# Kernel optimization log

Measured on AMD Instinct MI355X. Metric: run time of the kernel, lower is better.

## Reference

```python
import jax, jax.numpy as jnp
import numpy as np
from jax import lax

TAU = 0.1
LAMBDA_ABCD = 0.5
NUM_ANCHORS = 256
THRESH = 0.6
NEG_INF = -1e30


def sample_features(feat, anchors):
    # feat: [B,C,H,W], anchors: [B,N,2] in [0,1] (u,v). Bilinear, align_corners=False, zeros padding.
    B, C, H, W = feat.shape
    g = anchors * 2.0 - 1.0
    x = ((g[..., 0] + 1.0) * W - 1.0) / 2.0  # [B,N] pixel coords
    y = ((g[..., 1] + 1.0) * H - 1.0) / 2.0
    x0 = jnp.floor(x).astype(jnp.int32); x1 = x0 + 1
    y0 = jnp.floor(y).astype(jnp.int32); y1 = y0 + 1
    wx1 = x - x0.astype(x.dtype); wx0 = 1.0 - wx1
    wy1 = y - y0.astype(y.dtype); wy0 = 1.0 - wy1
    flat = feat.reshape(B, C, H * W)

    def gather(xi, yi):
        valid = ((xi >= 0) & (xi < W) & (yi >= 0) & (yi < H)).astype(feat.dtype)
        idx = jnp.clip(yi, 0, H - 1) * W + jnp.clip(xi, 0, W - 1)  # [B,N]
        v = jnp.take_along_axis(flat, idx[:, None, :], axis=2)  # [B,C,N]
        return v * valid[:, None, :]

    out = (gather(x0, y0) * (wx0 * wy0)[:, None, :]
           + gather(x1, y0) * (wx1 * wy0)[:, None, :]
           + gather(x0, y1) * (wx0 * wy1)[:, None, :]
           + gather(x1, y1) * (wx1 * wy1)[:, None, :])
    return out.transpose(0, 2, 1)  # [B,N,C]


def layer_norm(x, gamma, beta, eps=1e-5):
    mu = x.mean(-1, keepdims=True)
    var = ((x - mu) ** 2).mean(-1, keepdims=True)
    return (x - mu) * lax.rsqrt(var + eps) * gamma + beta


def l2norm(x, eps=1e-12):
    n = jnp.sqrt(jnp.sum(x * x, -1, keepdims=True))
    return x / jnp.maximum(n, eps)


def conv2d(x, w, b, pad):
    y = lax.conv_general_dilated(x, w, (1, 1), pad,
                                 dimension_numbers=('NCHW', 'OIHW', 'NCHW'))
    return y + b[None, :, None, None]


def setup_inputs() -> dict:
    key = jax.random.key(0)
    ks = jax.random.split(key, 12)
    B, Ct, Cs, H, W, P = 16, 1024, 512, 64, 64, 256
    s = lambda k, shp, fan: jax.random.normal(k, shp, jnp.float32) * (1.0 / np.sqrt(fan))
    return {
        'teacher_feat': jax.random.normal(ks[0], (B, Ct, H, W), jnp.float32),
        'student_feat': jax.random.normal(ks[1], (B, Cs, H, W), jnp.float32),
        'conv1_w': s(ks[2], (Ct // 2, Ct, 3, 3), Ct * 9),
        'conv1_b': jnp.zeros((Ct // 2,), jnp.float32),
        'conv2_w': s(ks[3], (1, Ct // 2, 1, 1), Ct // 2),
        'conv2_b': jnp.zeros((1,), jnp.float32),
        't_w': s(ks[4], (Ct, P), Ct), 't_b': jnp.zeros((P,), jnp.float32),
        't_g': jnp.ones((P,), jnp.float32), 't_beta': jnp.zeros((P,), jnp.float32),
        's_w': s(ks[5], (Cs, P), Cs), 's_b': jnp.zeros((P,), jnp.float32),
        's_g': jnp.ones((P,), jnp.float32), 's_beta': jnp.zeros((P,), jnp.float32),
    }


def reference(teacher_feat, student_feat, conv1_w, conv1_b, conv2_w, conv2_b,
              t_w, t_b, t_g, t_beta, s_w, s_b, s_g, s_beta):
    B, Ct, H, W = teacher_feat.shape
    # learnable anchor generator
    h = jax.nn.relu(conv2d(teacher_feat, conv1_w, conv1_b, 'SAME'))
    heatmap = jax.nn.softplus(conv2d(h, conv2_w, conv2_b, 'SAME'))  # [B,1,H,W]
    prob = heatmap.reshape(B, -1)
    prob = prob / (prob.sum(1, keepdims=True) + 1e-6)
    # multinomial without replacement via Gumbel top-k (fixed key -> deterministic)
    u01 = jax.random.uniform(jax.random.key(42), prob.shape, jnp.float32, 1e-8, 1.0)
    gumbel = -jnp.log(-jnp.log(u01))
    idx = lax.top_k(jnp.log(prob + 1e-12) + gumbel, NUM_ANCHORS)[1]  # [B,N]
    ax = (idx % W).astype(jnp.float32) / W
    ay = (idx // W).astype(jnp.float32) / H
    anchors = jnp.stack([ax, ay], -1)  # [B,N,2]

    ft = sample_features(teacher_feat, anchors)  # [B,N,Ct]
    fs = sample_features(student_feat, anchors)  # [B,N,Cs]
    ft = l2norm(layer_norm(jnp.einsum('bnc,cp->bnp', ft, t_w) + t_b, t_g, t_beta))
    fs = l2norm(layer_norm(jnp.einsum('bnc,cp->bnp', fs, s_w) + s_b, s_g, s_beta))

    loss_gafd = jnp.mean((fs - lax.stop_gradient(ft)) ** 2)

    saliency = sample_features(heatmap, anchors)[..., 0]  # [B,N]
    bd = saliency > THRESH * saliency.max(1, keepdims=True)  # [B,N] bool
    non_bd = ~bd

    pos = jnp.sum(fs * ft, -1) / TAU                       # [B,N]
    neg = jnp.einsum('bnc,bmc->bnm', fs, fs) / TAU          # [B,N,N]
    neg = jnp.where(non_bd[:, None, :], neg, NEG_INF)
    logits = jnp.concatenate([pos[..., None], neg], -1)    # [B,N,N+1]
    row_loss = jax.nn.logsumexp(logits, -1) - pos          # [B,N]

    bd_f = bd.astype(jnp.float32)
    cnt = bd_f.sum(1)
    per_b = (row_loss * bd_f).sum(1) / jnp.maximum(cnt, 1.0)
    valid = ((cnt > 0) & (non_bd.sum(1) > 0)).astype(jnp.float32)
    vnum = valid.sum()
    loss_abcd = jnp.where(vnum > 0, (per_b * valid).sum() / jnp.maximum(vnum, 1.0), 0.0)

    total_loss = loss_gafd + LAMBDA_ABCD * loss_abcd
    return total_loss, loss_gafd, loss_abcd, heatmap
```

## Files before the change

kernel.cpp:

```cpp
#include <hip/hip_runtime.h>
#include <stdint.h>


typedef float f32x4 __attribute__((ext_vector_type(4)));
typedef short s16x8 __attribute__((ext_vector_type(8)));

__device__ __forceinline__ unsigned short f2bf(float f) {
  unsigned u = __float_as_uint(f);
  u += 0x7fffu + ((u >> 16) & 1u);
  return (unsigned short)(u >> 16);
}
__device__ __forceinline__ float bf2f(unsigned short h) {
  return __uint_as_float((unsigned)h << 16);
}

__device__ __forceinline__ void gld16(const void* g, void* l) {
  __builtin_amdgcn_global_load_lds(
      (const __attribute__((address_space(1))) void*)g,
      (__attribute__((address_space(3))) void*)l, 16, 0, 0);
}

__device__ __forceinline__ float block_sum(float v, float* l4) {
  for (int m = 32; m; m >>= 1) v += __shfl_xor(v, m, 64);
  int wid = threadIdx.x >> 6;
  if ((threadIdx.x & 63) == 0) l4[wid] = v;
  __syncthreads();
  float r = l4[0] + l4[1] + l4[2] + l4[3];
  __syncthreads();
  return r;
}

__global__ void k_pad_transpose(const float* __restrict__ teacher,
                                unsigned short* __restrict__ tpad) {
  __shared__ __align__(16) unsigned short lds[64 * 65];
  int bid = blockIdx.x;
  int cb = bid & 15, y = (bid >> 4) & 63, b = bid >> 10;
  int t = threadIdx.x;
#pragma unroll
  for (int it = 0; it < 4; ++it) {
    int idx = it * 256 + t;
    int cl = idx >> 4, x4 = (idx & 15) * 4;
    float4 v = *(const float4*)&teacher[(size_t)(b * 1024 + cb * 64 + cl) * 4096 + y * 64 + x4];
    lds[cl * 65 + x4 + 0] = f2bf(v.x);
    lds[cl * 65 + x4 + 1] = f2bf(v.y);
    lds[cl * 65 + x4 + 2] = f2bf(v.z);
    lds[cl * 65 + x4 + 3] = f2bf(v.w);
  }
  __syncthreads();
  size_t obase = ((size_t)(b * 66 + y + 1) * 66 + 1) * 1024 + cb * 64;
#pragma unroll
  for (int it = 0; it < 2; ++it) {
    int wi = it * 256 + t;
    int x = wi >> 3, c0 = (wi & 7) * 8;
    s16x8 v;
#pragma unroll
    for (int k2 = 0; k2 < 8; ++k2) v[k2] = (short)lds[(c0 + k2) * 65 + x];
    *(s16x8*)(void*)&tpad[obase + (size_t)x * 1024 + c0] = v;
  }
  if (y == 0) {
    for (int idx = t; idx < 66 * 64; idx += 256) {
      int col = idx >> 6, cl = idx & 63;
      tpad[((size_t)(b * 66) * 66 + col) * 1024 + cb * 64 + cl] = 0;
    }
  }
  if (y == 63) {
    for (int idx = t; idx < 66 * 64; idx += 256) {
      int col = idx >> 6, cl = idx & 63;
      tpad[((size_t)(b * 66 + 65) * 66 + col) * 1024 + cb * 64 + cl] = 0;
    }
  }
  if (t < 128) {
    int col = (t >= 64) ? 65 : 0;
    int cl = t & 63;
    tpad[((size_t)(b * 66 + y + 1) * 66 + col) * 1024 + cb * 64 + cl] = 0;
  }
}

__global__ void k_wprep_all(const float* __restrict__ w1,
                            unsigned short* __restrict__ wt,
                            const float* __restrict__ tw, unsigned short* __restrict__ wTt,
                            const float* __restrict__ sw, unsigned short* __restrict__ wTs) {
  int blk = blockIdx.x, t = threadIdx.x;
  if (blk < 512) {
    __shared__ float wl[9216];
    int co = blk;
    const float* src = w1 + (size_t)co * 9216;
    for (int i = t; i < 9216; i += 256) wl[i] = src[i];
    __syncthreads();
    for (int i = t; i < 9216; i += 256) {
      int tap = i >> 10;
      int ci = i - (tap << 10);
      int kb = ci >> 6, kc = ci & 63;
      wt[(size_t)tap * 524288 + (size_t)kb * 32768 + co * 64 + kc] = f2bf(wl[ci * 9 + tap]);
    }
  } else if (blk < 1536) {
    int e = (blk - 512) * 256 + t;
    int p = e >> 10, k = e & 1023;
    wTt[e] = f2bf(tw[(size_t)k * 256 + p]);
  } else {
    int e = (blk - 1536) * 256 + t;
    int p = e >> 9, k = e & 511;
    wTs[e] = f2bf(sw[(size_t)k * 256 + p]);
  }
}

#define STAGE_A(buf, ts, h) do {                                              \
    int tap_ = (ts) >> 4, kb_ = (ts) & 15;                                    \
    int ky_ = tap_ / 3, kx_ = tap_ - ky_ * 3;                                 \
    unsigned o_ = (unsigned)(((ky_ * 66 + kx_) << 10) + (kb_ << 6));          \
    gld16(tpad + aoff[(h) * 2 + 0] + o_,                                      \
          (char*)(As[buf] + (((h) * 128 + wid * 8) << 6)));                   \
    gld16(tpad + aoff[(h) * 2 + 1] + o_,                                      \
          (char*)(As[buf] + (((h) * 128 + 64 + wid * 8) << 6)));              \
  } while (0)

#define STAGE_B(buf, ts, h) do {                                              \
    int tap_ = (ts) >> 4, kb_ = (ts) & 15;                                    \
    unsigned o_ = (unsigned)((tap_ << 19) + (kb_ << 15));                     \
    gld16(wt + boff[(h) * 2 + 0] + o_,                                        \
          (char*)(Bs[buf] + (((h) * 128 + wid * 8) << 6)));                   \
    gld16(wt + boff[(h) * 2 + 1] + o_,                                        \
          (char*)(Bs[buf] + (((h) * 128 + 64 + wid * 8) << 6)));              \
  } while (0)

#define LDA8(AF, buf, i0)                                                     \
  _Pragma("unroll") for (int i_ = 0; i_ < 4; ++i_)                            \
  _Pragma("unroll") for (int s_ = 0; s_ < 2; ++s_)                            \
    AF[i_][s_] = *(const s16x8*)(const void*)(                                \
        &As[buf][(wm * 128 + ((i0) + i_) * 16 + l15) * 64 +                   \
                 ((s_ * 4 + quad) ^ sw7) * 8]);

#define LDB4(BF, buf, j0)                                                     \
  _Pragma("unroll") for (int j_ = 0; j_ < 2; ++j_)                            \
  _Pragma("unroll") for (int s_ = 0; s_ < 2; ++s_)                            \
    BF[j_][s_] = *(const s16x8*)(const void*)(                                \
        &Bs[buf][(wn * 64 + ((j0) + j_) * 16 + l15) * 64 +                    \
                 ((s_ * 4 + quad) ^ sw7) * 8]);

#define MFMA16(AF, BF, i0, j0)                                                \
  _Pragma("unroll") for (int i_ = 0; i_ < 4; ++i_)                            \
  _Pragma("unroll") for (int j_ = 0; j_ < 2; ++j_)                            \
  _Pragma("unroll") for (int s_ = 0; s_ < 2; ++s_)                            \
    acc[(i0) + i_][(j0) + j_] = __builtin_amdgcn_mfma_f32_16x16x32_bf16(      \
        AF[i_][s_], BF[j_][s_], acc[(i0) + i_][(j0) + j_], 0, 0, 0);

#define PHASE_MID()                                                           \
  __builtin_amdgcn_s_barrier();                                               \
  asm volatile("s_waitcnt lgkmcnt(0)" ::: "memory");                          \
  __builtin_amdgcn_sched_barrier(0);                                          \
  __builtin_amdgcn_s_setprio(1)

#define PHASE_END()                                                           \
  __builtin_amdgcn_s_setprio(0);                                              \
  __builtin_amdgcn_sched_barrier(0);                                          \
  __builtin_amdgcn_s_barrier()

#define PHASE_END_VM()                                                        \
  __builtin_amdgcn_s_setprio(0);                                              \
  __builtin_amdgcn_sched_barrier(0);                                          \
  asm volatile("s_waitcnt vmcnt(4)" ::: "memory");                            \
  __builtin_amdgcn_s_barrier()

__global__ __launch_bounds__(512, 2) void k_conv(
    const unsigned short* __restrict__ tpad, const unsigned short* __restrict__ wt,
    const float* __restrict__ b1, const float* __restrict__ w2,
    float* __restrict__ heat) {
  __shared__ __align__(16) unsigned short As[2][256 * 64];
  __shared__ __align__(16) unsigned short Bs[2][256 * 64];
  int bid = blockIdx.x;
  int swz = (bid & 7) * 64 + (bid >> 3);
  int nt = swz & 1, mt = swz >> 1;
  int m0 = mt * 256, n0 = nt * 256;
  int t = threadIdx.x, wid = t >> 6, lane = t & 63;
  int wm = wid >> 2, wn = wid & 3;
  int quad = lane >> 4, l15 = lane & 15;
  int sw7 = l15 & 7;

  int srcChunk = (t & 7) ^ ((t >> 3) & 7);
  unsigned aoff[4], boff[4];
#pragma unroll
  for (int v = 0; v < 4; ++v) {
    int row = (v >> 1) * 128 + (v & 1) * 64 + (t >> 3);
    int m = m0 + row;
    int b = m >> 12, y = (m >> 6) & 63, x = m & 63;
    aoff[v] = (unsigned)((((b * 66 + y) * 66 + x) << 10) + srcChunk * 8);
    boff[v] = (unsigned)(((n0 + row) << 6) + srcChunk * 8);
  }

  f32x4 acc[8][4];
  const f32x4 fz = {0.f, 0.f, 0.f, 0.f};
#pragma unroll
  for (int i = 0; i < 8; ++i)
#pragma unroll
    for (int j = 0; j < 4; ++j) acc[i][j] = fz;

  STAGE_B(0, 0, 0); STAGE_B(0, 0, 1);
  STAGE_A(0, 0, 0); STAGE_A(0, 0, 1);
  STAGE_B(1, 1, 0); STAGE_B(1, 1, 1);
  asm volatile("s_waitcnt vmcnt(4)" ::: "memory");
  __builtin_amdgcn_s_barrier();

  for (int it2 = 0; it2 < 72; ++it2) {
    int T1 = it2 * 2 + 1;
    int tsA = (T1 + 1 <= 143) ? T1 + 1 : 143;
    int tsB = (T1 + 2 <= 143) ? T1 + 2 : 143;
    s16x8 af[4][2], bf01[2][2], bf23[2][2];
    LDA8(af, 0, 0);
    LDB4(bf01, 0, 0);
    STAGE_A(1, T1, 0);
    PHASE_MID();
    MFMA16(af, bf01, 0, 0);
    LDB4(bf23, 0, 2);
    PHASE_END();

    STAGE_A(1, T1, 1);
    PHASE_MID();
    MFMA16(af, bf23, 0, 2);
    LDA8(af, 0, 4);
    PHASE_END();

    STAGE_B(0, tsA, 0);
    PHASE_MID();
    MFMA16(af, bf01, 4, 0);
    PHASE_END();

    STAGE_B(0, tsA, 1);
    PHASE_MID();
    MFMA16(af, bf23, 4, 2);
    PHASE_END_VM();

    LDA8(af, 1, 0);
    LDB4(bf01, 1, 0);
    STAGE_A(0, tsA, 0);
    PHASE_MID();
    MFMA16(af, bf01, 0, 0);
    LDB4(bf23, 1, 2);
    PHASE_END();

    STAGE_A(0, tsA, 1);
    PHASE_MID();
    MFMA16(af, bf23, 0, 2);
    LDA8(af, 1, 4);
    PHASE_END();

    STAGE_B(1, tsB, 0);
    PHASE_MID();
    MFMA16(af, bf01, 4, 0);
    PHASE_END();

    STAGE_B(1, tsB, 1);
    PHASE_MID();
    MFMA16(af, bf23, 4, 2);
    PHASE_END_VM();
  }

  float w2v[4], b1v[4];
#pragma unroll
  for (int j = 0; j < 4; ++j) {
    int co = n0 + wn * 64 + j * 16 + l15;
    w2v[j] = w2[co];
    b1v[j] = b1[co];
  }
#pragma unroll
  for (int i = 0; i < 8; ++i) {
#pragma unroll
    for (int r = 0; r < 4; ++r) {
      float part = 0.f;
#pragma unroll
      for (int j = 0; j < 4; ++j) {
        float v = acc[i][j][r] + b1v[j];
        v = fmaxf(v, 0.f);
        part += v * w2v[j];
      }
#pragma unroll
      for (int msk = 1; msk < 16; msk <<= 1) part += __shfl_xor(part, msk, 64);
      if (l15 == 0) atomicAdd(&heat[m0 + wm * 128 + i * 16 + quad * 4 + r], part);
    }
  }
}

__device__ __forceinline__ unsigned rotl32(unsigned x, int d) {
  return (x << d) | (x >> (32 - d));
}
__device__ unsigned threefry_bits(unsigned lo) {
  const unsigned k0 = 0u, k1 = 42u;
  const unsigned k2 = 0x1BD11BDAu ^ k0 ^ k1;
  unsigned x0 = 0u + k0, x1 = lo + k1;
#define TF_R4(a, bq, c, d)                                \
  x0 += x1; x1 = rotl32(x1, a); x1 ^= x0;                 \
  x0 += x1; x1 = rotl32(x1, bq); x1 ^= x0;                \
  x0 += x1; x1 = rotl32(x1, c); x1 ^= x0;                 \
  x0 += x1; x1 = rotl32(x1, d); x1 ^= x0;
  TF_R4(13, 15, 26, 6)  x0 += k1; x1 += k2 + 1u;
  TF_R4(17, 29, 16, 24) x0 += k2; x1 += k0 + 2u;
  TF_R4(13, 15, 26, 6)  x0 += k0; x1 += k1 + 3u;
  TF_R4(17, 29, 16, 24) x0 += k1; x1 += k2 + 4u;
  TF_R4(13, 15, 26, 6)  x0 += k2; x1 += k0 + 5u;
#undef TF_R4
  return x0 ^ x1;
}

__global__ void k_score_topk_sal(const float* __restrict__ heat,
                                 const float* __restrict__ b2p,
                                 float* __restrict__ out_hm,
                                 int* __restrict__ idx_sel,
                                 int* __restrict__ bd, int* __restrict__ cnt,
                                 int* __restrict__ nbc) {
  __shared__ float hmp[4096];
  __shared__ unsigned keys[4096];
  __shared__ unsigned hist[256];
  __shared__ unsigned suf[256];
  __shared__ unsigned sel[2];
  __shared__ int wpos;
  __shared__ int idxl[256];
  __shared__ float l4[4];
  int b = blockIdx.x, t = threadIdx.x;
  float b2 = b2p[0];
  float lsum = 0.f;
#pragma unroll
  for (int j = 0; j < 16; ++j) {
    int e = j * 256 + t;
    float x = heat[b * 4096 + e] + b2;
    float sp = fmaxf(x, 0.f) + log1pf(expf(-fabsf(x)));
    hmp[e] = sp;
    lsum += sp;
  }
  float S = block_sum(lsum, l4);
  float denom = S + 1e-6f;
#pragma unroll
  for (int j = 0; j < 16; ++j) {
    int e = j * 256 + t;
    float sp = hmp[e];
    out_hm[b * 4096 + e] = sp;
    float lp = logf(sp / denom + 1e-12f);
    unsigned bits = threefry_bits((unsigned)(b * 4096 + e));
    float u01 = __uint_as_float((bits >> 9) | 0x3f800000u) - 1.0f;
    float u = fmaxf(1e-8f, u01 * (1.0f - 1e-8f) + 1e-8f);
    float gum = -logf(-logf(u));
    float sc = lp + gum;
    unsigned uu = __float_as_uint(sc);
    uu = (uu >> 31) ? ~uu : (uu | 0x80000000u);
    keys[e] = uu;
  }
  if (t == 0) wpos = 0;
  unsigned prefix = 0, hmask = 0, r = 256;
  for (int pass = 0; pass < 4; ++pass) {
    int shift = 24 - 8 * pass;
    hist[t] = 0;
    __syncthreads();
#pragma unroll
    for (int j = 0; j < 16; ++j) {
      unsigned u = keys[j * 256 + t];
      if ((u & hmask) == prefix) atomicAdd(&hist[(u >> shift) & 255u], 1u);
    }
    __syncthreads();
    suf[t] = hist[t];
    __syncthreads();
    for (int off = 1; off < 256; off <<= 1) {
      unsigned v = (t + off < 256) ? suf[t + off] : 0u;
      __syncthreads();
      suf[t] += v;
      __syncthreads();
    }
    unsigned above = (t < 255) ? suf[t + 1] : 0u;
    if (suf[t] >= r && above < r) {
      sel[0] = (unsigned)t;
      sel[1] = above;
    }
    __syncthreads();
    prefix |= sel[0] << shift;
    hmask |= 0xFFu << shift;
    r -= sel[1];
    __syncthreads();
  }
#pragma unroll
  for (int j = 0; j < 16; ++j) {
    int e = j * 256 + t;
    if (keys[e] > prefix) {
      int s = atomicAdd(&wpos, 1);
      idx_sel[b * 256 + s] = e;
      idxl[s] = e;
    }
  }
  __syncthreads();
#pragma unroll
  for (int j = 0; j < 16; ++j) {
    int e = j * 256 + t;
    if (keys[e] == prefix) {
      int s = atomicAdd(&wpos, 1);
      if (s < 256) {
        idx_sel[b * 256 + s] = e;
        idxl[s] = e;
      }
    }
  }
  __syncthreads();
  int idx = idxl[t];
  int px = idx & 63, py = idx >> 6;
  float v = 0.f;
  if (py > 0) {
    if (px > 0) v += hmp[(py - 1) * 64 + px - 1];
    v += hmp[(py - 1) * 64 + px];
  }
  if (px > 0) v += hmp[py * 64 + px - 1];
  v += hmp[py * 64 + px];
  float sal = 0.25f * v;
  float mx = sal;
  for (int m = 32; m; m >>= 1) mx = fmaxf(mx, __shfl_xor(mx, m, 64));
  if ((t & 63) == 0) l4[t >> 6] = mx;
  __syncthreads();
  mx = fmaxf(fmaxf(l4[0], l4[1]), fmaxf(l4[2], l4[3]));
  __syncthreads();
  int bdv = sal > 0.6f * mx ? 1 : 0;
  bd[b * 256 + t] = bdv;
  float c = block_sum((float)bdv, l4);
  if (t == 0) {
    cnt[b] = (int)c;
    nbc[b] = 256 - (int)c;
  }
}

__global__ void k_gather_t(const unsigned short* __restrict__ tpad,
                           const int* __restrict__ idx_sel,
                           unsigned short* __restrict__ ftb) {
  int t = threadIdx.x;
  int bn = blockIdx.x * 2 + (t >> 7);
  int tt = t & 127;
  int b = bn >> 8;
  int idx = idx_sel[bn];
  int px = idx & 63, py = idx >> 6;
  const unsigned short* base = tpad + ((size_t)(b * 66 + py) * 66 + px) * 1024 + tt * 8;
  s16x8 r0 = *(const s16x8*)(const void*)(base);
  s16x8 r1 = *(const s16x8*)(const void*)(base + 1024);
  s16x8 r2 = *(const s16x8*)(const void*)(base + 66 * 1024);
  s16x8 r3 = *(const s16x8*)(const void*)(base + 67 * 1024);
  s16x8 o;
#pragma unroll
  for (int k = 0; k < 8; ++k) {
    float v = bf2f((unsigned short)r0[k]) + bf2f((unsigned short)r1[k]) +
              bf2f((unsigned short)r2[k]) + bf2f((unsigned short)r3[k]);
    o[k] = (short)f2bf(0.25f * v);
  }
  *(s16x8*)(void*)&ftb[(size_t)bn * 1024 + tt * 8] = o;
}

__global__ void k_gather_s(const float* __restrict__ student,
                           const int* __restrict__ idx_sel,
                           unsigned short* __restrict__ fsbT) {
  __shared__ float plane[4096];
  int blk = blockIdx.x;
  int b = blk >> 9, c = blk & 511;
  int t = threadIdx.x;
  const float4* g4 = (const float4*)(student + ((size_t)b * 512 + c) * 4096);
  float4* p4 = (float4*)plane;
  for (int i = t; i < 1024; i += 256) p4[i] = g4[i];
  __syncthreads();
  int idx = idx_sel[b * 256 + t];
  int px = idx & 63, py = idx >> 6;
  float v = 0.f;
  if (py > 0) {
    if (px > 0) v += plane[(py - 1) * 64 + px - 1];
    v += plane[(py - 1) * 64 + px];
  }
  if (px > 0) v += plane[py * 64 + px - 1];
  v += plane[py * 64 + px];
  fsbT[((size_t)b * 512 + c) * 256 + t] = f2bf(0.25f * v);
}

__global__ void k_fsb_tr(const unsigned short* __restrict__ fsbT,
                         unsigned short* __restrict__ fsb) {
  __shared__ unsigned short tile[64][65];
  int blk = blockIdx.x;
  int b = blk >> 5, ct = (blk >> 2) & 7, nt = blk & 3;
  int t = threadIdx.x;
#pragma unroll
  for (int it = 0; it < 16; ++it) {
    int e = it * 256 + t;
    int cl = e >> 6, n = e & 63;
    tile[cl][n] = fsbT[((size_t)(b * 512 + ct * 64 + cl)) * 256 + nt * 64 + n];
  }
  __syncthreads();
#pragma unroll
  for (int it = 0; it < 16; ++it) {
    int e = it * 256 + t;
    int n = e >> 6, cl = e & 63;
    fsb[((size_t)(b * 256 + nt * 64 + n)) * 512 + ct * 64 + cl] = tile[cl][n];
  }
}

__global__ __launch_bounds__(256) void k_proj_both(
    const unsigned short* __restrict__ At, const unsigned short* __restrict__ Wtt,
    const unsigned short* __restrict__ Asrc, const unsigned short* __restrict__ Wts,
    float* __restrict__ outt, float* __restrict__ outs) {
  __shared__ __align__(16) unsigned short Al[128 * 64];
  __shared__ __align__(16) unsigned short Bl[128 * 64];
  int g = blockIdx.x;
  const unsigned short* A;
  const unsigned short* Wt;
  float* outp;
  int K, bid;
  if (g < 64) { A = At; Wt = Wtt; outp = outt; K = 1024; bid = g; }
  else        { A = Asrc; Wt = Wts; outp = outs; K = 512; bid = g - 64; }
  int nt = bid & 1, mt = bid >> 1;
  int m0 = mt * 128, n0 = nt * 128;
  int t = threadIdx.x, wid = t >> 6, lane = t & 63;
  int wm = wid & 1, wn = wid >> 1;
  int quad = lane >> 4, l15 = lane & 15;

  f32x4 acc[4][4];
  const f32x4 fz = {0.f, 0.f, 0.f, 0.f};
#pragma unroll
  for (int i = 0; i < 4; ++i)
#pragma unroll
    for (int j = 0; j < 4; ++j) acc[i][j] = fz;

  int row4[4];
#pragma unroll
  for (int jj = 0; jj < 4; ++jj) row4[jj] = (wid * 4 + jj) * 8 + (lane >> 3);
  int kcol = (lane & 7) * 8;

  int nkb = K >> 6;
  for (int kb = 0; kb < nkb; ++kb) {
#pragma unroll
    for (int jj = 0; jj < 4; ++jj) {
      gld16(A + (size_t)(m0 + row4[jj]) * K + kb * 64 + kcol,
            (char*)Al + (wid * 4 + jj) * 1024);
      gld16(Wt + (size_t)(n0 + row4[jj]) * K + kb * 64 + kcol,
            (char*)Bl + (wid * 4 + jj) * 1024);
    }
    __syncthreads();
#pragma unroll
    for (int s = 0; s < 2; ++s) {
      s16x8 af[4], bf[4];
#pragma unroll
      for (int i = 0; i < 4; ++i) {
        af[i] = *(const s16x8*)(const void*)(Al + (wm * 64 + i * 16 + l15) * 64 + s * 32 + quad * 8);
        bf[i] = *(const s16x8*)(const void*)(Bl + (wn * 64 + i * 16 + l15) * 64 + s * 32 + quad * 8);
      }
#pragma unroll
      for (int i = 0; i < 4; ++i)
#pragma unroll
        for (int j = 0; j < 4; ++j)
          acc[i][j] = __builtin_amdgcn_mfma_f32_16x16x32_bf16(af[i], bf[j], acc[i][j], 0, 0, 0);
    }
    __syncthreads();
  }
#pragma unroll
  for (int i = 0; i < 4; ++i)
#pragma unroll
    for (int j = 0; j < 4; ++j)
#pragma unroll
      for (int r = 0; r < 4; ++r) {
        int m = m0 + wm * 64 + i * 16 + quad * 4 + r;
        int p = n0 + wn * 64 + j * 16 + l15;
        outp[(size_t)m * 256 + p] = acc[i][j][r];
      }
}

__global__ void k_ln(const float* __restrict__ projp, const float* __restrict__ bias,
                     const float* __restrict__ g, const float* __restrict__ beta,
                     float* __restrict__ outf) {
  __shared__ float l4[4];
  int row = blockIdx.x, t = threadIdx.x;
  float x = projp[(size_t)row * 256 + t] + bias[t];
  float s1 = block_sum(x, l4);
  float mu = s1 * (1.f / 256.f);
  float d = x - mu;
  float s2 = block_sum(d * d, l4);
  float rstd = rsqrtf(s2 * (1.f / 256.f) + 1e-5f);
  float xn = d * rstd * g[t] + beta[t];
  float ss = block_sum(xn * xn, l4);
  float o = xn / fmaxf(sqrtf(ss), 1e-12f);
  outf[(size_t)row * 256 + t] = o;
}

__global__ void k_ln_s_pos(const float* __restrict__ projp, const float* __restrict__ bias,
                           const float* __restrict__ g, const float* __restrict__ beta,
                           const float* __restrict__ ftn,
                           float* __restrict__ outf, unsigned short* __restrict__ outb,
                           float* __restrict__ pos, float* __restrict__ gsum) {
  __shared__ float l4[4];
  int row = blockIdx.x, t = threadIdx.x;
  float x = projp[(size_t)row * 256 + t] + bias[t];
  float s1 = block_sum(x, l4);
  float mu = s1 * (1.f / 256.f);
  float d = x - mu;
  float s2 = block_sum(d * d, l4);
  float rstd = rsqrtf(s2 * (1.f / 256.f) + 1e-5f);
  float xn = d * rstd * g[t] + beta[t];
  float ss = block_sum(xn * xn, l4);
  float o = xn / fmaxf(sqrtf(ss), 1e-12f);
  outf[(size_t)row * 256 + t] = o;
  outb[(size_t)row * 256 + t] = f2bf(o);
  float bt = ftn[(size_t)row * 256 + t];
  float sdot = block_sum(o * bt, l4);
  if (t == 0) pos[row] = sdot * 10.f;
  float dd = o - bt;
  float ssq = block_sum(dd * dd, l4);
  if (t == 0) atomicAdd(gsum, ssq);
}

__global__ __launch_bounds__(256) void k_abcd_rows(
    const unsigned short* __restrict__ fsnb, const int* __restrict__ bd,
    const float* __restrict__ pos, float* __restrict__ rowloss) {
  __shared__ __align__(16) unsigned short Ab[64 * 64];
  __shared__ __align__(16) unsigned short Bb[256 * 64];
  __shared__ float mrg[64][4][2];
  int b = blockIdx.x >> 2, nb = blockIdx.x & 3;
  int n0 = nb * 64;
  int t = threadIdx.x, w = t >> 6, lane = t & 63, quad = lane >> 4, l15 = lane & 15;
  f32x4 acc[4][4];
  const f32x4 fz = {0.f, 0.f, 0.f, 0.f};
#pragma unroll
  for (int i = 0; i < 4; ++i)
#pragma unroll
    for (int j = 0; j < 4; ++j) acc[i][j] = fz;
  const unsigned short* fb = fsnb + (size_t)b * 256 * 256;

  for (int kc = 0; kc < 4; ++kc) {
    {
      int r = t >> 2, cc = (t & 3) * 16;
      const uint4* s = (const uint4*)(const void*)(fb + (size_t)(n0 + r) * 256 + kc * 64 + cc);
      *(uint4*)(void*)(Ab + r * 64 + cc) = s[0];
      *(uint4*)(void*)(Ab + r * 64 + cc + 8) = s[1];
    }
#pragma unroll
    for (int it = 0; it < 4; ++it) {
      int m = it * 64 + (t >> 2), cc = (t & 3) * 16;
      const uint4* s = (const uint4*)(const void*)(fb + (size_t)m * 256 + kc * 64 + cc);
      *(uint4*)(void*)(Bb + m * 64 + cc) = s[0];
      *(uint4*)(void*)(Bb + m * 64 + cc + 8) = s[1];
    }
    __syncthreads();
#pragma unroll
    for (int s = 0; s < 2; ++s) {
      s16x8 af[4], bf[4];
#pragma unroll
      for (int i = 0; i < 4; ++i) {
        af[i] = *(const s16x8*)(const void*)(Ab + (i * 16 + l15) * 64 + s * 32 + quad * 8);
        bf[i] = *(const s16x8*)(const void*)(Bb + (w * 64 + i * 16 + l15) * 64 + s * 32 + quad * 8);
      }
#pragma unroll
      for (int i = 0; i < 4; ++i)
#pragma unroll
        for (int j = 0; j < 4; ++j)
          acc[i][j] = __builtin_amdgcn_mfma_f32_16x16x32_bf16(af[i], bf[j], acc[i][j], 0, 0, 0);
    }
    __syncthreads();
  }

  int nbmask[4];
#pragma unroll
  for (int j = 0; j < 4; ++j) nbmask[j] = bd[b * 256 + w * 64 + j * 16 + l15];
#pragma unroll
  for (int i = 0; i < 4; ++i) {
#pragma unroll
    for (int r = 0; r < 4; ++r) {
      float mxv = -1e30f, se = 0.f;
#pragma unroll
      for (int j = 0; j < 4; ++j) {
        float v = nbmask[j] ? -1e30f : (acc[i][j][r] / 0.1f);
        if (v > mxv) {
          se = se * expf(mxv - v) + 1.f;
          mxv = v;
        } else {
          se += expf(v - mxv);
        }
      }
#pragma unroll
      for (int msk = 1; msk < 16; msk <<= 1) {
        float omx = __shfl_xor(mxv, msk, 64);
        float ose = __shfl_xor(se, msk, 64);
        float nm = fmaxf(mxv, omx);
        se = se * expf(mxv - nm) + ose * expf(omx - nm);
        mxv = nm;
      }
      if (l15 == 0) {
        mrg[i * 16 + quad * 4 + r][w][0] = mxv;
        mrg[i * 16 + quad * 4 + r][w][1] = se;
      }
    }
  }
  __syncthreads();
  if (t < 64) {
    float MX = -1e30f, SE = 0.f;
    for (int ww = 0; ww < 4; ++ww) {
      float omx = mrg[t][ww][0], ose = mrg[t][ww][1];
      float nm = fmaxf(MX, omx);
      SE = SE * expf(MX - nm) + ose * expf(omx - nm);
      MX = nm;
    }
    float p = pos[b * 256 + n0 + t];
    float nm = fmaxf(MX, p);
    float se2 = SE * expf(MX - nm) + expf(p - nm);
    rowloss[b * 256 + n0 + t] = nm + logf(se2) - p;
  }
}

__global__ void k_final(const float* __restrict__ gsum, const float* __restrict__ rowloss,
                        const int* __restrict__ bd, const int* __restrict__ cnt,
                        const int* __restrict__ nbc, float* __restrict__ out) {
  __shared__ float l4[4];
  int t = threadIdx.x;
  float abcd_acc = 0.f, vnum = 0.f;
  for (int b = 0; b < 16; ++b) {
    float c = bd[b * 256 + t] ? rowloss[b * 256 + t] : 0.f;
    float s = block_sum(c, l4);
    if (t == 0) {
      float cb = (float)cnt[b];
      float per = s / fmaxf(cb, 1.f);
      if (cnt[b] > 0 && nbc[b] > 0) {
        abcd_acc += per;
        vnum += 1.f;
      }
    }
  }
  if (t == 0) {
    float gafd = gsum[0] / 1048576.f;
    float abcd = vnum > 0.f ? abcd_acc / fmaxf(vnum, 1.f) : 0.f;
    out[0] = gafd + 0.5f * abcd;
    out[1] = gafd;
    out[2] = abcd;
  }
}

static constexpr size_t OFF_TPAD = 0;
static constexpr size_t TPAD_BYTES = (size_t)16 * 66 * 66 * 1024 * 2;
static constexpr size_t OFF_WT = OFF_TPAD + TPAD_BYTES;
static constexpr size_t WT_BYTES = (size_t)9 * 16 * 512 * 64 * 2;
static constexpr size_t OFF_HEAT = OFF_WT + WT_BYTES;
static constexpr size_t OFF_GSUM = OFF_HEAT + 262144;
static constexpr size_t OFF_HM = OFF_GSUM + 256;
static constexpr size_t OFF_SC = OFF_HM + 262144;
static constexpr size_t OFF_IDX = OFF_SC + 262144;
static constexpr size_t OFF_FTB = OFF_IDX + 16384;
static constexpr size_t OFF_FSB = OFF_FTB + (size_t)4096 * 1024 * 2;
static constexpr size_t OFF_FSBT = OFF_FSB + (size_t)4096 * 512 * 2;
static constexpr size_t OFF_WTT = OFF_FSBT + (size_t)4096 * 512 * 2;
static constexpr size_t OFF_WTS = OFF_WTT + (size_t)256 * 1024 * 2;
static constexpr size_t OFF_PRT = OFF_WTS + (size_t)256 * 512 * 2;
static constexpr size_t OFF_PRS = OFF_PRT + (size_t)4096 * 256 * 4;
static constexpr size_t OFF_FTN = OFF_PRS + (size_t)4096 * 256 * 4;
static constexpr size_t OFF_FSN = OFF_FTN + (size_t)4096 * 256 * 4;
static constexpr size_t OFF_FSNB = OFF_FSN + (size_t)4096 * 256 * 4;
static constexpr size_t OFF_POS = OFF_FSNB + (size_t)4096 * 256 * 2;
static constexpr size_t OFF_BD = OFF_POS + 16384;
static constexpr size_t OFF_CNT = OFF_BD + 16384;
static constexpr size_t OFF_NBC = OFF_CNT + 64;
static constexpr size_t OFF_RL = OFF_NBC + 64;

extern "C" void kernel_launch(void* const* d_in, const int* in_sizes, int n_in,
                              void* d_out, int out_size, void* d_ws, size_t ws_size,
                              hipStream_t stream) {
  const float* teacher = (const float*)d_in[0];
  const float* student = (const float*)d_in[1];
  const float* w1 = (const float*)d_in[2];
  const float* b1 = (const float*)d_in[3];
  const float* w2 = (const float*)d_in[4];
  const float* b2 = (const float*)d_in[5];
  const float* t_w = (const float*)d_in[6];
  const float* t_b = (const float*)d_in[7];
  const float* t_g = (const float*)d_in[8];
  const float* t_be = (const float*)d_in[9];
  const float* s_w = (const float*)d_in[10];
  const float* s_b = (const float*)d_in[11];
  const float* s_g = (const float*)d_in[12];
  const float* s_be = (const float*)d_in[13];
  float* out = (float*)d_out;

  char* ws = (char*)d_ws;
  unsigned short* tpad = (unsigned short*)(ws + OFF_TPAD);
  unsigned short* wt = (unsigned short*)(ws + OFF_WT);
  float* heat = (float*)(ws + OFF_HEAT);
  float* gsum = (float*)(ws + OFF_GSUM);
  int* idx_sel = (int*)(ws + OFF_IDX);
  unsigned short* ftb = (unsigned short*)(ws + OFF_FTB);
  unsigned short* fsb = (unsigned short*)(ws + OFF_FSB);
  unsigned short* fsbT = (unsigned short*)(ws + OFF_FSBT);
  unsigned short* wTt = (unsigned short*)(ws + OFF_WTT);
  unsigned short* wTs = (unsigned short*)(ws + OFF_WTS);
  float* projt = (float*)(ws + OFF_PRT);
  float* projs = (float*)(ws + OFF_PRS);
  float* ftn = (float*)(ws + OFF_FTN);
  float* fsn = (float*)(ws + OFF_FSN);
  unsigned short* fsnb = (unsigned short*)(ws + OFF_FSNB);
  float* pos = (float*)(ws + OFF_POS);
  int* bd = (int*)(ws + OFF_BD);
  int* cnt = (int*)(ws + OFF_CNT);
  int* nbc = (int*)(ws + OFF_NBC);
  float* rowloss = (float*)(ws + OFF_RL);

  hipMemsetAsync(ws + OFF_HEAT, 0, 262144 + 256, stream);

  k_pad_transpose<<<16384, 256, 0, stream>>>(teacher, tpad);
  k_wprep_all<<<2048, 256, 0, stream>>>(w1, wt, t_w, wTt, s_w, wTs);
  k_conv<<<512, 512, 0, stream>>>(tpad, wt, b1, w2, heat);
  k_score_topk_sal<<<16, 256, 0, stream>>>(heat, b2, out + 3, idx_sel, bd, cnt, nbc);
  k_gather_t<<<2048, 256, 0, stream>>>(tpad, idx_sel, ftb);
  k_gather_s<<<8192, 256, 0, stream>>>(student, idx_sel, fsbT);
  k_fsb_tr<<<512, 256, 0, stream>>>(fsbT, fsb);
  k_proj_both<<<128, 256, 0, stream>>>(ftb, wTt, fsb, wTs, projt, projs);
  k_ln<<<4096, 256, 0, stream>>>(projt, t_b, t_g, t_be, ftn);
  k_ln_s_pos<<<4096, 256, 0, stream>>>(projs, s_b, s_g, s_be, ftn, fsn, fsnb, pos, gsum);
  k_abcd_rows<<<64, 256, 0, stream>>>(fsnb, bd, pos, rowloss);
  k_final<<<1, 256, 0, stream>>>(gsum, rowloss, bd, cnt, nbc, out);
}
```

Measured before the change: 1.144 ms.

## Merge pad and weight-prep kernels, reschedule conv loop, warp-scan histogram, split abcd rows

Fuses the teacher pad/transpose and weight-prep kernels into a single launch that shares one LDS buffer, removing one kernel launch. In the conv main loop, the A-stage loads are issued before the LDS reads, with sched_barrier and setprio hints replacing one PHASE_MID. The top-k histogram suffix sum switches from a barrier-heavy LDS scan to a wave-shuffle scan. The ABCD row kernel uses 32-row tiles over twice as many blocks to raise parallelism, at the cost of reloading the B tile more often.

```diff
diff --git a/kernel.cpp b/kernel.cpp
--- a/kernel.cpp
+++ b/kernel.cpp
@@ -30,60 +30,58 @@
   return r;
 }
 
-__global__ void k_pad_transpose(const float* __restrict__ teacher,
-                                unsigned short* __restrict__ tpad) {
-  __shared__ __align__(16) unsigned short lds[64 * 65];
-  int bid = blockIdx.x;
-  int cb = bid & 15, y = (bid >> 4) & 63, b = bid >> 10;
-  int t = threadIdx.x;
-#pragma unroll
-  for (int it = 0; it < 4; ++it) {
-    int idx = it * 256 + t;
-    int cl = idx >> 4, x4 = (idx & 15) * 4;
-    float4 v = *(const float4*)&teacher[(size_t)(b * 1024 + cb * 64 + cl) * 4096 + y * 64 + x4];
-    lds[cl * 65 + x4 + 0] = f2bf(v.x);
-    lds[cl * 65 + x4 + 1] = f2bf(v.y);
-    lds[cl * 65 + x4 + 2] = f2bf(v.z);
-    lds[cl * 65 + x4 + 3] = f2bf(v.w);
-  }
-  __syncthreads();
-  size_t obase = ((size_t)(b * 66 + y + 1) * 66 + 1) * 1024 + cb * 64;
-#pragma unroll
-  for (int it = 0; it < 2; ++it) {
-    int wi = it * 256 + t;
-    int x = wi >> 3, c0 = (wi & 7) * 8;
-    s16x8 v;
-#pragma unroll
-    for (int k2 = 0; k2 < 8; ++k2) v[k2] = (short)lds[(c0 + k2) * 65 + x];
-    *(s16x8*)(void*)&tpad[obase + (size_t)x * 1024 + c0] = v;
-  }
-  if (y == 0) {
-    for (int idx = t; idx < 66 * 64; idx += 256) {
-      int col = idx >> 6, cl = idx & 63;
-      tpad[((size_t)(b * 66) * 66 + col) * 1024 + cb * 64 + cl] = 0;
-    }
-  }
-  if (y == 63) {
-    for (int idx = t; idx < 66 * 64; idx += 256) {
-      int col = idx >> 6, cl = idx & 63;
-      tpad[((size_t)(b * 66 + 65) * 66 + col) * 1024 + cb * 64 + cl] = 0;
-    }
-  }
-  if (t < 128) {
-    int col = (t >= 64) ? 65 : 0;
-    int cl = t & 63;
-    tpad[((size_t)(b * 66 + y + 1) * 66 + col) * 1024 + cb * 64 + cl] = 0;
-  }
-}
-
-__global__ void k_wprep_all(const float* __restrict__ w1,
+__global__ void k_pad_wprep(const float* __restrict__ teacher,
+                            unsigned short* __restrict__ tpad,
+                            const float* __restrict__ w1,
                             unsigned short* __restrict__ wt,
                             const float* __restrict__ tw, unsigned short* __restrict__ wTt,
                             const float* __restrict__ sw, unsigned short* __restrict__ wTs) {
+  __shared__ __align__(16) char smem[36864];
   int blk = blockIdx.x, t = threadIdx.x;
-  if (blk < 512) {
-    __shared__ float wl[9216];
-    int co = blk;
+  if (blk < 16384) {
+    unsigned short* lds = (unsigned short*)smem;
+    int cb = blk & 15, y = (blk >> 4) & 63, b = blk >> 10;
+#pragma unroll
+    for (int it = 0; it < 4; ++it) {
+      int idx = it * 256 + t;
+      int cl = idx >> 4, x4 = (idx & 15) * 4;
+      float4 v = *(const float4*)&teacher[(size_t)(b * 1024 + cb * 64 + cl) * 4096 + y * 64 + x4];
+      lds[cl * 65 + x4 + 0] = f2bf(v.x);
+      lds[cl * 65 + x4 + 1] = f2bf(v.y);
+      lds[cl * 65 + x4 + 2] = f2bf(v.z);
+      lds[cl * 65 + x4 + 3] = f2bf(v.w);
+    }
+    __syncthreads();
+    size_t obase = ((size_t)(b * 66 + y + 1) * 66 + 1) * 1024 + cb * 64;
+#pragma unroll
+    for (int it = 0; it < 2; ++it) {
+      int wi = it * 256 + t;
+      int x = wi >> 3, c0 = (wi & 7) * 8;
+      s16x8 v;
+#pragma unroll
+      for (int k2 = 0; k2 < 8; ++k2) v[k2] = (short)lds[(c0 + k2) * 65 + x];
+      *(s16x8*)(void*)&tpad[obase + (size_t)x * 1024 + c0] = v;
+    }
+    if (y == 0) {
+      for (int idx = t; idx < 66 * 64; idx += 256) {
+        int col = idx >> 6, cl = idx & 63;
+        tpad[((size_t)(b * 66) * 66 + col) * 1024 + cb * 64 + cl] = 0;
+      }
+    }
+    if (y == 63) {
+      for (int idx = t; idx < 66 * 64; idx += 256) {
+        int col = idx >> 6, cl = idx & 63;
+        tpad[((size_t)(b * 66 + 65) * 66 + col) * 1024 + cb * 64 + cl] = 0;
+      }
+    }
+    if (t < 128) {
+      int col = (t >= 64) ? 65 : 0;
+      int cl = t & 63;
+      tpad[((size_t)(b * 66 + y + 1) * 66 + col) * 1024 + cb * 64 + cl] = 0;
+    }
+  } else if (blk < 16896) {
+    float* wl = (float*)smem;
+    int co = blk - 16384;
     const float* src = w1 + (size_t)co * 9216;
     for (int i = t; i < 9216; i += 256) wl[i] = src[i];
     __syncthreads();
@@ -93,12 +91,12 @@
       int kb = ci >> 6, kc = ci & 63;
       wt[(size_t)tap * 524288 + (size_t)kb * 32768 + co * 64 + kc] = f2bf(wl[ci * 9 + tap]);
     }
-  } else if (blk < 1536) {
-    int e = (blk - 512) * 256 + t;
+  } else if (blk < 17920) {
+    int e = (blk - 16896) * 256 + t;
     int p = e >> 10, k = e & 1023;
     wTt[e] = f2bf(tw[(size_t)k * 256 + p]);
   } else {
-    int e = (blk - 1536) * 256 + t;
+    int e = (blk - 17920) * 256 + t;
     int p = e >> 9, k = e & 511;
     wTs[e] = f2bf(sw[(size_t)k * 256 + p]);
   }
@@ -205,10 +203,12 @@
     int tsA = (T1 + 1 <= 143) ? T1 + 1 : 143;
     int tsB = (T1 + 2 <= 143) ? T1 + 2 : 143;
     s16x8 af[4][2], bf01[2][2], bf23[2][2];
+
+    __builtin_amdgcn_sched_barrier(0);
+    STAGE_A(1, T1, 0);
     LDA8(af, 0, 0);
     LDB4(bf01, 0, 0);
-    STAGE_A(1, T1, 0);
-    PHASE_MID();
+    __builtin_amdgcn_s_setprio(1);
     MFMA16(af, bf01, 0, 0);
     LDB4(bf23, 0, 2);
     PHASE_END();
@@ -229,10 +229,11 @@
     MFMA16(af, bf23, 4, 2);
     PHASE_END_VM();
 
+    __builtin_amdgcn_sched_barrier(0);
+    STAGE_A(0, tsA, 0);
     LDA8(af, 1, 0);
     LDB4(bf01, 1, 0);
-    STAGE_A(0, tsA, 0);
-    PHASE_MID();
+    __builtin_amdgcn_s_setprio(1);
     MFMA16(af, bf01, 0, 0);
     LDB4(bf23, 1, 2);
     PHASE_END();
@@ -310,6 +311,7 @@
   __shared__ unsigned keys[4096];
   __shared__ unsigned hist[256];
   __shared__ unsigned suf[256];
+  __shared__ unsigned wsum[4];
   __shared__ unsigned sel[2];
   __shared__ int wpos;
   __shared__ int idxl[256];
@@ -354,14 +356,17 @@
       if ((u & hmask) == prefix) atomicAdd(&hist[(u >> shift) & 255u], 1u);
     }
     __syncthreads();
-    suf[t] = hist[t];
-    __syncthreads();
-    for (int off = 1; off < 256; off <<= 1) {
-      unsigned v = (t + off < 256) ? suf[t + off] : 0u;
-      __syncthreads();
-      suf[t] += v;
-      __syncthreads();
-    }
+    unsigned v = hist[t];
+#pragma unroll
+    for (int off = 1; off < 64; off <<= 1) {
+      unsigned o = __shfl_down(v, off, 64);
+      if ((t & 63) + off < 64) v += o;
+    }
+    if ((t & 63) == 0) wsum[t >> 6] = v;
+    __syncthreads();
+    for (int ww = (t >> 6) + 1; ww < 4; ++ww) v += wsum[ww];
+    suf[t] = v;
+    __syncthreads();
     unsigned above = (t < 255) ? suf[t + 1] : 0u;
     if (suf[t] >= r && above < r) {
       sel[0] = (unsigned)t;
@@ -603,26 +608,25 @@
 __global__ __launch_bounds__(256) void k_abcd_rows(
     const unsigned short* __restrict__ fsnb, const int* __restrict__ bd,
     const float* __restrict__ pos, float* __restrict__ rowloss) {
-  __shared__ __align__(16) unsigned short Ab[64 * 64];
+  __shared__ __align__(16) unsigned short Ab[32 * 64];
   __shared__ __align__(16) unsigned short Bb[256 * 64];
-  __shared__ float mrg[64][4][2];
-  int b = blockIdx.x >> 2, nb = blockIdx.x & 3;
-  int n0 = nb * 64;
+  __shared__ float mrg[32][4][2];
+  int b = blockIdx.x >> 3, nb = blockIdx.x & 7;
+  int n0 = nb * 32;
   int t = threadIdx.x, w = t >> 6, lane = t & 63, quad = lane >> 4, l15 = lane & 15;
-  f32x4 acc[4][4];
+  f32x4 acc[2][4];
   const f32x4 fz = {0.f, 0.f, 0.f, 0.f};
 #pragma unroll
-  for (int i = 0; i < 4; ++i)
+  for (int i = 0; i < 2; ++i)
 #pragma unroll
     for (int j = 0; j < 4; ++j) acc[i][j] = fz;
   const unsigned short* fb = fsnb + (size_t)b * 256 * 256;
 
   for (int kc = 0; kc < 4; ++kc) {
     {
-      int r = t >> 2, cc = (t & 3) * 16;
-      const uint4* s = (const uint4*)(const void*)(fb + (size_t)(n0 + r) * 256 + kc * 64 + cc);
-      *(uint4*)(void*)(Ab + r * 64 + cc) = s[0];
-      *(uint4*)(void*)(Ab + r * 64 + cc + 8) = s[1];
+      int r = t >> 3, cc = (t & 7) * 8;
+      *(uint4*)(void*)(Ab + r * 64 + cc) =
+          *(const uint4*)(const void*)(fb + (size_t)(n0 + r) * 256 + kc * 64 + cc);
     }
 #pragma unroll
     for (int it = 0; it < 4; ++it) {
@@ -634,14 +638,15 @@
     __syncthreads();
 #pragma unroll
     for (int s = 0; s < 2; ++s) {
-      s16x8 af[4], bf[4];
-#pragma unroll
-      for (int i = 0; i < 4; ++i) {
+      s16x8 af[2], bf[4];
+#pragma unroll
+      for (int i = 0; i < 2; ++i)
         af[i] = *(const s16x8*)(const void*)(Ab + (i * 16 + l15) * 64 + s * 32 + quad * 8);
-        bf[i] = *(const s16x8*)(const void*)(Bb + (w * 64 + i * 16 + l15) * 64 + s * 32 + quad * 8);
-      }
-#pragma unroll
-      for (int i = 0; i < 4; ++i)
+#pragma unroll
+      for (int j = 0; j < 4; ++j)
+        bf[j] = *(const s16x8*)(const void*)(Bb + (w * 64 + j * 16 + l15) * 64 + s * 32 + quad * 8);
+#pragma unroll
+      for (int i = 0; i < 2; ++i)
 #pragma unroll
         for (int j = 0; j < 4; ++j)
           acc[i][j] = __builtin_amdgcn_mfma_f32_16x16x32_bf16(af[i], bf[j], acc[i][j], 0, 0, 0);
@@ -653,7 +658,7 @@
 #pragma unroll
   for (int j = 0; j < 4; ++j) nbmask[j] = bd[b * 256 + w * 64 + j * 16 + l15];
 #pragma unroll
-  for (int i = 0; i < 4; ++i) {
+  for (int i = 0; i < 2; ++i) {
 #pragma unroll
     for (int r = 0; r < 4; ++r) {
       float mxv = -1e30f, se = 0.f;
@@ -682,7 +687,7 @@
     }
   }
   __syncthreads();
-  if (t < 64) {
+  if (t < 32) {
     float MX = -1e30f, SE = 0.f;
     for (int ww = 0; ww < 4; ++ww) {
       float omx = mrg[t][ww][0], ose = mrg[t][ww][1];
@@ -792,8 +797,7 @@
 
   hipMemsetAsync(ws + OFF_HEAT, 0, 262144 + 256, stream);
 
-  k_pad_transpose<<<16384, 256, 0, stream>>>(teacher, tpad);
-  k_wprep_all<<<2048, 256, 0, stream>>>(w1, wt, t_w, wTt, s_w, wTs);
+  k_pad_wprep<<<18432, 256, 0, stream>>>(teacher, tpad, w1, wt, t_w, wTt, s_w, wTs);
   k_conv<<<512, 512, 0, stream>>>(tpad, wt, b1, w2, heat);
   k_score_topk_sal<<<16, 256, 0, stream>>>(heat, b2, out + 3, idx_sel, bd, cnt, nbc);
   k_gather_t<<<2048, 256, 0, stream>>>(tpad, idx_sel, ftb);
@@ -802,6 +806,6 @@
   k_proj_both<<<128, 256, 0, stream>>>(ftb, wTt, fsb, wTs, projt, projs);
   k_ln<<<4096, 256, 0, stream>>>(projt, t_b, t_g, t_be, ftn);
   k_ln_s_pos<<<4096, 256, 0, stream>>>(projs, s_b, s_g, s_be, ftn, fsn, fsnb, pos, gsum);
-  k_abcd_rows<<<64, 256, 0, stream>>>(fsnb, bd, pos, rowloss);
+  k_abcd_rows<<<128, 256, 0, stream>>>(fsnb, bd, pos, rowloss);
   k_final<<<1, 256, 0, stream>>>(gsum, rowloss, bd, cnt, nbc, out);
 }
```

New measurement: 1.162 ms. No clear change (+1.6%).
